# Optimization experiments

Measured on AMD Instinct MI355X. Metric: run time of the kernel, lower is better.

The kernel has to match this reference:

```python
import jax, jax.numpy as jnp
import numpy as np

EPS = 1e-6


def _segment_mean(x, seg, num_segments):
    # x: [N, ...] -> [num_segments, ...] mean over nodes of each segment
    sums = jax.ops.segment_sum(x, seg, num_segments=num_segments)
    ones = jnp.ones((x.shape[0],) + (1,) * (x.ndim - 1), x.dtype)
    cnts = jax.ops.segment_sum(ones, seg, num_segments=num_segments)
    return sums / jnp.maximum(cnts, 1.0)


def setup_inputs() -> dict:
    key = jax.random.key(0)
    k1, k2, k3 = jax.random.split(key, 3)
    N, SDIM, VDIM, B = 500000, 128, 64, 1024
    s = jax.random.normal(k1, (N, SDIM), dtype=jnp.float32)
    v = jax.random.normal(k2, (N, 3, VDIM), dtype=jnp.float32)
    weight_s = jnp.ones((SDIM,), dtype=jnp.float32)
    bias_s = jnp.zeros((SDIM,), dtype=jnp.float32)
    batch = jnp.sort(jax.random.randint(k3, (N,), 0, B, dtype=jnp.int32))
    return {"s": s, "v": v, "weight_s": weight_s, "bias_s": bias_s,
            "batch": batch, "num_segments": B}


def reference(s, v, weight_s, bias_s, batch, num_segments):
    # scalar branch: per-graph mean/var over all node features in the graph
    smean = s.mean(axis=-1, keepdims=True)                      # [N,1]
    smean = _segment_mean(smean, batch, num_segments)           # [B,1]
    sc = s - smean[batch]                                       # [N,sdim]
    var = (sc * sc).mean(axis=-1, keepdims=True)                # [N,1]
    var = jnp.maximum(_segment_mean(var, batch, num_segments), EPS)  # [B,1]
    sout = sc / var[batch] * weight_s + bias_s                  # NOTE: divide by var (not sqrt), as in source

    # vector branch: per-graph mean squared vector norm
    vmean = (v * v).sum(axis=1, keepdims=True).mean(axis=-1, keepdims=True)  # [N,1,1]
    vmean = jnp.maximum(_segment_mean(vmean, batch, num_segments), EPS)      # [B,1,1]
    vout = v / vmean[batch]
    return sout, vout
```

## Files before the change

### kernel.cpp

```cpp
#include <hip/hip_runtime.h>


#define MAIN_THREADS 1024
#define MAIN_GRID 256
#define EPS 1e-6f

typedef float vfloat4 __attribute__((ext_vector_type(4)));

__device__ __forceinline__ int lower_bound_i(const int* __restrict__ a, int n, int val) {
    int lo = 0, hi = n;
    while (lo < hi) {
        int mid = (lo + hi) >> 1;
        if (a[mid] < val) lo = mid + 1; else hi = mid;
    }
    return lo;
}

__device__ __forceinline__ void nt_store4(float4* p, float4 x) {
    vfloat4 r; r.x = x.x; r.y = x.y; r.z = x.z; r.w = x.w;
    __builtin_nontemporal_store(r, reinterpret_cast<vfloat4*>(p));
}

__global__ void eln_boundaries(const int* __restrict__ batch, int N,
                               int* __restrict__ off, int capB) {
    const int Beff = batch[N - 1] + 1;
    const int stride = gridDim.x * blockDim.x;
    for (int g = blockIdx.x * blockDim.x + threadIdx.x; g <= Beff; g += stride) {
        if (g <= capB) off[g] = lower_bound_i(batch, N, g);
    }
}

__global__ __launch_bounds__(MAIN_THREADS) void eln_fused(
    const float* __restrict__ s, const float* __restrict__ v,
    const float* __restrict__ wgt, const float* __restrict__ bia,
    const int* __restrict__ batch, const int* __restrict__ off, int capB,
    float* __restrict__ souts, float* __restrict__ vouts, int N)
{
    const int Beff = batch[N - 1] + 1;
    const bool use_off = (off != nullptr) && (Beff <= capB);

    __shared__ float red[MAIN_THREADS / 64][3];
    __shared__ float stats[3];

    const int tid  = threadIdx.x;
    const int lane = tid & 63;
    const int wid  = tid >> 6;

    const float4* s4 = reinterpret_cast<const float4*>(s);
    const float4* v4 = reinterpret_cast<const float4*>(v);
    float4* so4 = reinterpret_cast<float4*>(souts);
    float4* vo4 = reinterpret_cast<float4*>(vouts);

    const float4 w4 = reinterpret_cast<const float4*>(wgt)[tid & 31];
    const float4 b4 = reinterpret_cast<const float4*>(bia)[tid & 31];

    for (int g = blockIdx.x; g < Beff; g += gridDim.x) {
        int start, end;
        if (use_off) {
            start = off[g];
            end   = off[g + 1];
        } else {
            start = lower_bound_i(batch, N, g);
            end   = lower_bound_i(batch, N, g + 1);
        }
        const int cnt = end - start;

        float sum_s = 0.f, sum_s2 = 0.f, sum_v2 = 0.f;
        const int s_lo = start * 32 + tid, s_hi = end * 32;
        const int v_lo = start * 48 + tid, v_hi = end * 48;
        #pragma unroll 8
        for (int i = s_lo; i < s_hi; i += MAIN_THREADS) {
            float4 x = s4[i];
            sum_s  += (x.x + x.y) + (x.z + x.w);
            sum_s2 += x.x * x.x + x.y * x.y + x.z * x.z + x.w * x.w;
        }
        #pragma unroll 8
        for (int i = v_lo; i < v_hi; i += MAIN_THREADS) {
            float4 x = v4[i];
            sum_v2 += x.x * x.x + x.y * x.y + x.z * x.z + x.w * x.w;
        }
        #pragma unroll
        for (int o = 32; o > 0; o >>= 1) {
            sum_s  += __shfl_down(sum_s,  o, 64);
            sum_s2 += __shfl_down(sum_s2, o, 64);
            sum_v2 += __shfl_down(sum_v2, o, 64);
        }
        if (lane == 0) {
            red[wid][0] = sum_s; red[wid][1] = sum_s2; red[wid][2] = sum_v2;
        }
        __syncthreads();
        if (tid == 0) {
            float ts = 0.f, ts2 = 0.f, tv2 = 0.f;
            #pragma unroll
            for (int w = 0; w < MAIN_THREADS / 64; ++w) {
                ts += red[w][0]; ts2 += red[w][1]; tv2 += red[w][2];
            }
            const float fc    = fmaxf((float)cnt, 1.0f);
            const float invns = 1.0f / (128.0f * fc);
            const float gmean = ts * invns;
            const float gvar  = fmaxf(ts2 * invns - gmean * gmean, EPS);
            const float gvm   = fmaxf(tv2 / (64.0f * fc), EPS);
            stats[0] = gmean;
            stats[1] = 1.0f / gvar;
            stats[2] = 1.0f / gvm;
        }
        __syncthreads();
        const float gmean = stats[0], ivar = stats[1], ivm = stats[2];

        #pragma unroll 4
        for (int i = s_lo; i < s_hi; i += MAIN_THREADS) {
            float4 x = s4[i];
            float4 o;
            o.x = (x.x - gmean) * ivar * w4.x + b4.x;
            o.y = (x.y - gmean) * ivar * w4.y + b4.y;
            o.z = (x.z - gmean) * ivar * w4.z + b4.z;
            o.w = (x.w - gmean) * ivar * w4.w + b4.w;
            nt_store4(&so4[i], o);
        }
        #pragma unroll 4
        for (int i = v_lo; i < v_hi; i += MAIN_THREADS) {
            float4 x = v4[i];
            float4 o;
            o.x = x.x * ivm; o.y = x.y * ivm; o.z = x.z * ivm; o.w = x.w * ivm;
            nt_store4(&vo4[i], o);
        }
    }
}

extern "C" void kernel_launch(void* const* d_in, const int* in_sizes, int n_in,
                              void* d_out, int out_size, void* d_ws, size_t ws_size,
                              hipStream_t stream) {
    const float* s   = (const float*)d_in[0];
    const float* v   = (const float*)d_in[1];
    const float* wgt = (const float*)d_in[2];
    const float* bia = (const float*)d_in[3];
    const int*   bat = (const int*)d_in[4];
    const int N = in_sizes[4];

    float* souts = (float*)d_out;
    float* vouts = souts + (size_t)N * 128;

    int* off = nullptr;
    int capB = -1;
    if (ws_size >= 4 * 4200) {
        off  = (int*)d_ws;
        capB = (int)(ws_size / 4) - 2;
        if (capB > 1 << 20) capB = 1 << 20;
        eln_boundaries<<<16, 256, 0, stream>>>(bat, N, off, capB);
    }

    eln_fused<<<MAIN_GRID, MAIN_THREADS, 0, stream>>>(
        s, v, wgt, bia, bat, off, capB, souts, vouts, N);
}
```

Measured before the change: 1.076 ms.

## Split fused per-graph kernel into stats pass and flat elementwise normalize pass

Replaces the single per-segment kernel (one block per graph, reading data twice) with two kernels. The first computes per-graph mean, inverse variance and inverse vector norm into a workspace array. The second is a flat grid-stride elementwise pass that looks up each node's stats through batch. It walks chunks in reverse order so it may hit data still cached from the first pass. This removes the load imbalance from uneven graph sizes and raises occupancy. The costs are an extra kernel launch, a per-element batch/stats gather, and no fallback when the workspace is too small.

```diff
diff --git a/kernel.cpp b/kernel.cpp
--- a/kernel.cpp
+++ b/kernel.cpp
@@ -1,8 +1,12 @@
 #include <hip/hip_runtime.h>
 
 
-#define MAIN_THREADS 1024
-#define MAIN_GRID 256
+#define K1_THREADS 256
+#define K1_GRID    1024
+#define K2_THREADS 256
+#define K2_SBLK    1024
+#define K2_VBLK    1536
+#define K2_UNROLL  8
 #define EPS 1e-6f
 
 typedef float vfloat4 __attribute__((ext_vector_type(4)));
@@ -21,108 +25,123 @@
     __builtin_nontemporal_store(r, reinterpret_cast<vfloat4*>(p));
 }
 
-__global__ void eln_boundaries(const int* __restrict__ batch, int N,
-                               int* __restrict__ off, int capB) {
+__global__ __launch_bounds__(K1_THREADS) void eln_stats(
+    const float* __restrict__ s, const float* __restrict__ v,
+    const int* __restrict__ batch, float4* __restrict__ stats,
+    int N, int statCap)
+{
+    __shared__ int sh_se[2];
+    __shared__ float red[K1_THREADS / 64][3];
+
     const int Beff = batch[N - 1] + 1;
-    const int stride = gridDim.x * blockDim.x;
-    for (int g = blockIdx.x * blockDim.x + threadIdx.x; g <= Beff; g += stride) {
-        if (g <= capB) off[g] = lower_bound_i(batch, N, g);
-    }
-}
-
-__global__ __launch_bounds__(MAIN_THREADS) void eln_fused(
-    const float* __restrict__ s, const float* __restrict__ v,
-    const float* __restrict__ wgt, const float* __restrict__ bia,
-    const int* __restrict__ batch, const int* __restrict__ off, int capB,
-    float* __restrict__ souts, float* __restrict__ vouts, int N)
-{
-    const int Beff = batch[N - 1] + 1;
-    const bool use_off = (off != nullptr) && (Beff <= capB);
-
-    __shared__ float red[MAIN_THREADS / 64][3];
-    __shared__ float stats[3];
-
     const int tid  = threadIdx.x;
     const int lane = tid & 63;
     const int wid  = tid >> 6;
 
     const float4* s4 = reinterpret_cast<const float4*>(s);
     const float4* v4 = reinterpret_cast<const float4*>(v);
-    float4* so4 = reinterpret_cast<float4*>(souts);
-    float4* vo4 = reinterpret_cast<float4*>(vouts);
 
-    const float4 w4 = reinterpret_cast<const float4*>(wgt)[tid & 31];
-    const float4 b4 = reinterpret_cast<const float4*>(bia)[tid & 31];
+    for (int g = blockIdx.x; g < Beff && g < statCap; g += gridDim.x) {
+        if (tid < 2) sh_se[tid] = lower_bound_i(batch, N, g + tid);
+        __syncthreads();
+        const int start = sh_se[0], end = sh_se[1];
 
-    for (int g = blockIdx.x; g < Beff; g += gridDim.x) {
-        int start, end;
-        if (use_off) {
-            start = off[g];
-            end   = off[g + 1];
-        } else {
-            start = lower_bound_i(batch, N, g);
-            end   = lower_bound_i(batch, N, g + 1);
-        }
-        const int cnt = end - start;
-
-        float sum_s = 0.f, sum_s2 = 0.f, sum_v2 = 0.f;
-        const int s_lo = start * 32 + tid, s_hi = end * 32;
-        const int v_lo = start * 48 + tid, v_hi = end * 48;
+        float ss = 0.f, ss2 = 0.f, sv2 = 0.f;
+        const int s_hi = end * 32;
+        const int v_hi = end * 48;
         #pragma unroll 8
-        for (int i = s_lo; i < s_hi; i += MAIN_THREADS) {
+        for (int i = start * 32 + tid; i < s_hi; i += K1_THREADS) {
             float4 x = s4[i];
-            sum_s  += (x.x + x.y) + (x.z + x.w);
-            sum_s2 += x.x * x.x + x.y * x.y + x.z * x.z + x.w * x.w;
+            ss  += (x.x + x.y) + (x.z + x.w);
+            ss2 += x.x * x.x + x.y * x.y + x.z * x.z + x.w * x.w;
         }
         #pragma unroll 8
-        for (int i = v_lo; i < v_hi; i += MAIN_THREADS) {
+        for (int i = start * 48 + tid; i < v_hi; i += K1_THREADS) {
             float4 x = v4[i];
-            sum_v2 += x.x * x.x + x.y * x.y + x.z * x.z + x.w * x.w;
+            sv2 += x.x * x.x + x.y * x.y + x.z * x.z + x.w * x.w;
         }
         #pragma unroll
         for (int o = 32; o > 0; o >>= 1) {
-            sum_s  += __shfl_down(sum_s,  o, 64);
-            sum_s2 += __shfl_down(sum_s2, o, 64);
-            sum_v2 += __shfl_down(sum_v2, o, 64);
+            ss  += __shfl_down(ss,  o, 64);
+            ss2 += __shfl_down(ss2, o, 64);
+            sv2 += __shfl_down(sv2, o, 64);
         }
-        if (lane == 0) {
-            red[wid][0] = sum_s; red[wid][1] = sum_s2; red[wid][2] = sum_v2;
-        }
+        if (lane == 0) { red[wid][0] = ss; red[wid][1] = ss2; red[wid][2] = sv2; }
         __syncthreads();
         if (tid == 0) {
             float ts = 0.f, ts2 = 0.f, tv2 = 0.f;
             #pragma unroll
-            for (int w = 0; w < MAIN_THREADS / 64; ++w) {
+            for (int w = 0; w < K1_THREADS / 64; ++w) {
                 ts += red[w][0]; ts2 += red[w][1]; tv2 += red[w][2];
             }
-            const float fc    = fmaxf((float)cnt, 1.0f);
+            const float fc    = fmaxf((float)(end - start), 1.0f);
             const float invns = 1.0f / (128.0f * fc);
             const float gmean = ts * invns;
             const float gvar  = fmaxf(ts2 * invns - gmean * gmean, EPS);
             const float gvm   = fmaxf(tv2 / (64.0f * fc), EPS);
-            stats[0] = gmean;
-            stats[1] = 1.0f / gvar;
-            stats[2] = 1.0f / gvm;
+            stats[g] = make_float4(gmean, 1.0f / gvar, 1.0f / gvm, 0.0f);
         }
         __syncthreads();
-        const float gmean = stats[0], ivar = stats[1], ivm = stats[2];
+    }
+}
 
-        #pragma unroll 4
-        for (int i = s_lo; i < s_hi; i += MAIN_THREADS) {
-            float4 x = s4[i];
-            float4 o;
-            o.x = (x.x - gmean) * ivar * w4.x + b4.x;
-            o.y = (x.y - gmean) * ivar * w4.y + b4.y;
-            o.z = (x.z - gmean) * ivar * w4.z + b4.z;
-            o.w = (x.w - gmean) * ivar * w4.w + b4.w;
-            nt_store4(&so4[i], o);
+__global__ __launch_bounds__(K2_THREADS) void eln_norm(
+    const float* __restrict__ s, const float* __restrict__ v,
+    const float* __restrict__ wgt, const float* __restrict__ bia,
+    const int* __restrict__ batch, const float4* __restrict__ stats,
+    float* __restrict__ souts, float* __restrict__ vouts, int N)
+{
+    const int tid = threadIdx.x;
+    const int CH  = K2_THREADS * K2_UNROLL;
+
+    if (blockIdx.x < K2_SBLK) {
+        const float4* s4  = reinterpret_cast<const float4*>(s);
+        float4*       so4 = reinterpret_cast<float4*>(souts);
+        const float4* w4t = reinterpret_cast<const float4*>(wgt);
+        const float4* b4t = reinterpret_cast<const float4*>(bia);
+        const int total = N * 32;
+        const int nch   = (total + CH - 1) / CH;
+        for (int c = blockIdx.x; c < nch; c += K2_SBLK) {
+            const int base = (nch - 1 - c) * CH + tid;
+            #pragma unroll
+            for (int u = 0; u < K2_UNROLL; ++u) {
+                const int i = base + u * K2_THREADS;
+                if (i < total) {
+                    float4 x = s4[i];
+                    const int node = i >> 5;
+                    const int col  = i & 31;
+                    const float4 st = stats[batch[node]];
+                    const float4 w  = w4t[col];
+                    const float4 b  = b4t[col];
+                    float4 o;
+                    o.x = (x.x - st.x) * st.y * w.x + b.x;
+                    o.y = (x.y - st.x) * st.y * w.y + b.y;
+                    o.z = (x.z - st.x) * st.y * w.z + b.z;
+                    o.w = (x.w - st.x) * st.y * w.w + b.w;
+                    nt_store4(&so4[i], o);
+                }
+            }
         }
-        #pragma unroll 4
-        for (int i = v_lo; i < v_hi; i += MAIN_THREADS) {
-            float4 x = v4[i];
-            float4 o;
-            o.x = x.x * ivm; o.y = x.y * ivm; o.z = x.z * ivm; o.w = x.w * ivm;
-            nt_store4(&vo4[i], o);
+    } else {
+        const float4* v4  = reinterpret_cast<const float4*>(v);
+        float4*       vo4 = reinterpret_cast<float4*>(vouts);
+        const int total = N * 48;
+        const int nch   = (total + CH - 1) / CH;
+        for (int c = blockIdx.x - K2_SBLK; c < nch; c += K2_VBLK) {
+            const int base = (nch - 1 - c) * CH + tid;
+            #pragma unroll
+            for (int u = 0; u < K2_UNROLL; ++u) {
+                const int i = base + u * K2_THREADS;
+                if (i < total) {
+                    float4 x = v4[i];
+                    const int node = i / 48;
+                    const float ivm = stats[batch[node]].z;
+                    float4 o;
+                    o.x = x.x * ivm; o.y = x.y * ivm;
+                    o.z = x.z * ivm; o.w = x.w * ivm;
+                    nt_store4(&vo4[i], o);
+                }
+            }
         }
     }
 }
@@ -140,15 +159,11 @@
     float* souts = (float*)d_out;
     float* vouts = souts + (size_t)N * 128;
 
-    int* off = nullptr;
-    int capB = -1;
-    if (ws_size >= 4 * 4200) {
-        off  = (int*)d_ws;
-        capB = (int)(ws_size / 4) - 2;
-        if (capB > 1 << 20) capB = 1 << 20;
-        eln_boundaries<<<16, 256, 0, stream>>>(bat, N, off, capB);
-    }
+    float4* stats = (float4*)d_ws;
+    int statCap = (int)(ws_size / sizeof(float4));
+    if (statCap > (1 << 24)) statCap = 1 << 24;
 
-    eln_fused<<<MAIN_GRID, MAIN_THREADS, 0, stream>>>(
-        s, v, wgt, bia, bat, off, capB, souts, vouts, N);
+    eln_stats<<<K1_GRID, K1_THREADS, 0, stream>>>(s, v, bat, stats, N, statCap);
+    eln_norm<<<K2_SBLK + K2_VBLK, K2_THREADS, 0, stream>>>(
+        s, v, wgt, bia, bat, stats, souts, vouts, N);
 }
```

Measured after the change: 1.143 ms. 6.2% more time.
